# Kernel optimization log

Measured on AMD Instinct MI355X. Metric: run time of the kernel, lower is better.

## Reference

```python
import jax, jax.numpy as jnp
import numpy as np

N_NODES = 100000


def _mean_agg(x, src, dst, n_nodes):
    # mean of src-node features over in-edges of each dst node (DGL copy_u + mean)
    summed = jax.ops.segment_sum(x[src], dst, num_segments=n_nodes)  # [N, F]
    deg = jax.ops.segment_sum(jnp.ones_like(src, dtype=x.dtype), dst, num_segments=n_nodes)
    return summed / jnp.maximum(deg, 1.0)[:, None]  # nodes w/o in-edges -> 0


def _sage_conv(x, src, dst, W_self, W_neigh, b):
    # DGL SAGEConv('mean'): fc_self(h) + fc_neigh(mean_neigh(h)) + bias
    h_neigh = _mean_agg(x, src, dst, x.shape[0])
    return x @ W_self + h_neigh @ W_neigh + b


def setup_inputs() -> dict:
    key = jax.random.key(0)
    ks = jax.random.split(key, 8)
    F_IN, F_H, E = 128, 128, 1600000
    s = 1.0 / np.sqrt(F_IN)
    return {
        "x": jax.random.normal(ks[0], (N_NODES, F_IN), dtype=jnp.float32),
        "src": jax.random.randint(ks[1], (E,), 0, N_NODES, dtype=jnp.int64),
        "dst": jax.random.randint(ks[2], (E,), 0, N_NODES, dtype=jnp.int64),
        "W1_self": jax.random.normal(ks[3], (F_IN, F_H), dtype=jnp.float32) * s,
        "W1_neigh": jax.random.normal(ks[4], (F_IN, F_H), dtype=jnp.float32) * s,
        "b1": jnp.zeros((F_H,), dtype=jnp.float32),
        "W2_self": jax.random.normal(ks[5], (F_H, F_H), dtype=jnp.float32) * s,
        "W2_neigh": jax.random.normal(ks[6], (F_H, F_H), dtype=jnp.float32) * s,
        "b2": jnp.zeros((F_H,), dtype=jnp.float32),
    }


def reference(x, src, dst, W1_self, W1_neigh, b1, W2_self, W2_neigh, b2):
    h = _sage_conv(x, src, dst, W1_self, W1_neigh, b1)
    # dropout in eval mode == identity
    h = jax.nn.relu(h)
    return _sage_conv(h, src, dst, W2_self, W2_neigh, b2)
```

## Files before the change

### kernel.cpp

```cpp
#include <hip/hip_runtime.h>

#define F 128
#define NN 100000
#define NBUK 782
#define NBLK 256
#define LD 136
#define N4 (NN * F / 4)
#define N4A (N4 / 2)
#define SORT_CAP 8192

typedef __attribute__((ext_vector_type(8))) short short8;
typedef __attribute__((ext_vector_type(4))) float f32x4;
typedef __attribute__((ext_vector_type(2))) float f32x2;
typedef __attribute__((ext_vector_type(4))) int int4v;
typedef __attribute__((ext_vector_type(2))) int int2v;
typedef __attribute__((ext_vector_type(4))) unsigned short us4;
typedef unsigned short ushort_t;
typedef unsigned char uchar_t;

__device__ __forceinline__ ushort_t f2b(float f) {
    union { float f; unsigned u; } x;
    x.f = f;
    unsigned r = x.u + 0x7fffu + ((x.u >> 16) & 1u);
    return (ushort_t)(r >> 16);
}
__device__ __forceinline__ float b2f(ushort_t u) {
    union { unsigned u; float f; } x;
    x.u = ((unsigned)u) << 16;
    return x.f;
}

__device__ __forceinline__ unsigned f_to_e4m3(float v) {
    union { float f; unsigned b; } x; x.f = v;
    unsigned s = (x.b >> 24) & 0x80u;
    float a = fabsf(v);
    if (!(a < 448.f)) return s | 0x7Eu;
    if (a < 0.015625f) return s | (unsigned)__float2int_rn(a * 512.f);
    unsigned ab = x.b & 0x7FFFFFFFu;
    unsigned r = ab + 0x7FFFFu + ((ab >> 20) & 1u);
    unsigned e = (r >> 23) - 120u;
    return s | ((e << 3) | ((r >> 20) & 7u));
}
__device__ __forceinline__ float e4m3_to_f(unsigned u) {
    unsigned s = (u & 0x80u) << 24;
    unsigned e = (u >> 3) & 15u;
    unsigned m = u & 7u;
    union { unsigned b; float f; } x;
    x.b = s | ((e + 120u) << 23) | (m << 20);
    float f = x.f;
    if (e == 0) f = fmaf(f, 2.f, s ? 0.015625f : -0.015625f);
    return f;
}
__device__ __forceinline__ unsigned pack4_fp8(float f0, float f1, float f2, float f3) {
#if __has_builtin(__builtin_amdgcn_cvt_pk_fp8_f32)
    int w = 0;
    w = __builtin_amdgcn_cvt_pk_fp8_f32(f0, f1, w, false);
    w = __builtin_amdgcn_cvt_pk_fp8_f32(f2, f3, w, true);
    return (unsigned)w;
#else
    return f_to_e4m3(f0) | (f_to_e4m3(f1) << 8) | (f_to_e4m3(f2) << 16) |
           (f_to_e4m3(f3) << 24);
#endif
}
__device__ __forceinline__ void dec4(int w, float* o) {
#if __has_builtin(__builtin_amdgcn_cvt_pk_f32_fp8)
    f32x2 a = __builtin_amdgcn_cvt_pk_f32_fp8(w, false);
    f32x2 b = __builtin_amdgcn_cvt_pk_f32_fp8(w, true);
    o[0] = a[0]; o[1] = a[1]; o[2] = b[0]; o[3] = b[1];
#else
    o[0] = e4m3_to_f((unsigned)w & 0xFFu);
    o[1] = e4m3_to_f(((unsigned)w >> 8) & 0xFFu);
    o[2] = e4m3_to_f(((unsigned)w >> 16) & 0xFFu);
    o[3] = e4m3_to_f(((unsigned)w >> 24) & 0xFFu);
#endif
}

__device__ __forceinline__ int4v ld_row16(const ushort_t* p) {
    int4v r;
    asm volatile("global_load_dwordx4 %0, %1, off" : "=v"(r) : "v"(p) : "memory");
    return r;
}
__device__ __forceinline__ int2v ld_row8(const uchar_t* p) {
    int2v r;
    asm volatile("global_load_dwordx2 %0, %1, off" : "=v"(r) : "v"(p) : "memory");
    return r;
}

__global__ __launch_bounds__(256) void k1_fused(
    const int* __restrict__ dst, int* __restrict__ H, int E, int chunk,
    const float* __restrict__ Wa, const float* __restrict__ Wb,
    const float* __restrict__ Wc, const float* __restrict__ Wd,
    ushort_t* __restrict__ Oa, ushort_t* __restrict__ Ob,
    ushort_t* __restrict__ Oc, ushort_t* __restrict__ Od,
    const float* __restrict__ X, ushort_t* __restrict__ Y,
    uchar_t* __restrict__ X8) {
    __shared__ union {
        int h[NBUK];
        float tile[32][33];
    } u;
    const int blk = blockIdx.x;
    if (blk < NBLK) {
        for (int i = threadIdx.x; i < NBUK; i += 256) u.h[i] = 0;
        __syncthreads();
        const int s0 = blk * chunk, s1 = min(E, s0 + chunk);
        for (int i = s0 + threadIdx.x; i < s1; i += 256)
            atomicAdd(&u.h[dst[i] >> 7], 1);
        __syncthreads();
        for (int i = threadIdx.x; i < NBUK; i += 256)
            H[blk * NBUK + i] = u.h[i];
    } else if (blk < NBLK + 64) {
        const int m = (blk - NBLK) >> 4;
        const int b = (blk - NBLK) & 15;
        const float* W = (m == 0) ? Wa : (m == 1) ? Wb : (m == 2) ? Wc : Wd;
        ushort_t* WT = (m == 0) ? Oa : (m == 1) ? Ob : (m == 2) ? Oc : Od;
        const int by = (b >> 2) * 32;
        const int bx = (b & 3) * 32;
        const int tx = threadIdx.x & 31, ty = threadIdx.x >> 5;
        for (int i = 0; i < 32; i += 8)
            u.tile[ty + i][tx] = W[(by + ty + i) * F + bx + tx];
        __syncthreads();
        for (int i = 0; i < 32; i += 8)
            WT[(bx + ty + i) * F + by + tx] = f2b(u.tile[tx][ty + i]);
    } else {
        const int i = (blk - NBLK - 64) * 256 + threadIdx.x;
        if (i < N4A) {
            float4 v = ((const float4*)X)[i];
            us4 o;
            o.x = f2b(v.x); o.y = f2b(v.y); o.z = f2b(v.z); o.w = f2b(v.w);
            ((us4*)Y)[i] = o;
            ((unsigned*)X8)[i] = pack4_fp8(v.x, v.y, v.z, v.w);
        }
    }
}

__global__ __launch_bounds__(256) void scan_cols(int* __restrict__ H,
                                                 int* __restrict__ Htot) {
    __shared__ int s[NBLK];
    const int k = blockIdx.x;
    const int t = threadIdx.x;
    const int v = H[t * NBUK + k];
    s[t] = v;
    __syncthreads();
    for (int d = 1; d < NBLK; d <<= 1) {
        const int u = (t >= d) ? s[t - d] : 0;
        __syncthreads();
        s[t] += u;
        __syncthreads();
    }
    H[t * NBUK + k] = s[t] - v;
    if (t == NBLK - 1) Htot[k] = s[t];
}

__global__ __launch_bounds__(1024) void k2_fused(
    const int* __restrict__ Htot, int* __restrict__ boffs, int E,
    const float* __restrict__ X, ushort_t* __restrict__ Y,
    uchar_t* __restrict__ X8) {
    if (blockIdx.x == 0) {
        __shared__ int tot[1024];
        const int k = threadIdx.x;
        const int v = (k < NBUK) ? Htot[k] : 0;
        tot[k] = v;
        __syncthreads();
        for (int d = 1; d < 1024; d <<= 1) {
            const int u = (k >= d) ? tot[k - d] : 0;
            __syncthreads();
            tot[k] += u;
            __syncthreads();
        }
        if (k < NBUK) boffs[k] = tot[k] - v;
        if (k == 0) boffs[NBUK] = E;
    } else {
        const int i = N4A + (blockIdx.x - 1) * 1024 + threadIdx.x;
        if (i < N4) {
            float4 v = ((const float4*)X)[i];
            us4 o;
            o.x = f2b(v.x); o.y = f2b(v.y); o.z = f2b(v.z); o.w = f2b(v.w);
            ((us4*)Y)[i] = o;
            ((unsigned*)X8)[i] = pack4_fp8(v.x, v.y, v.z, v.w);
        }
    }
}

__global__ __launch_bounds__(256) void scatter2(const int* __restrict__ src,
                                                const int* __restrict__ dst,
                                                const int* __restrict__ H,
                                                const int* __restrict__ boffs,
                                                unsigned* __restrict__ pairs,
                                                int E, int chunk) {
    __shared__ int cur[NBUK];
    const int b = blockIdx.x;
    for (int i = threadIdx.x; i < NBUK; i += 256)
        cur[i] = boffs[i] + H[b * NBUK + i];
    __syncthreads();
    const int s0 = b * chunk, s1 = min(E, s0 + chunk);
    for (int i = s0 + threadIdx.x; i < s1; i += 256) {
        const int d = dst[i];
        const int p = atomicAdd(&cur[d >> 7], 1);
        pairs[p] = ((unsigned)(d & 127) << 20) | (unsigned)src[i];
    }
}

__global__ __launch_bounds__(256) void bucket_sort(const unsigned* __restrict__ pairs,
                                                   const int* __restrict__ boffs,
                                                   int* __restrict__ offs,
                                                   int* __restrict__ csr) {
    __shared__ int cnt[128], loffs[128], lcur[128];
    __shared__ unsigned sbuf[SORT_CAP];
    const int b = blockIdx.x, t = threadIdx.x;
    const int e0 = boffs[b], e1 = boffs[b + 1];
    const int n = e1 - e0;
    const int node0 = b << 7;
    const int nnode = min(128, NN - node0);
    if (t < 128) cnt[t] = 0;
    __syncthreads();
    for (int i = e0 + t; i < e1; i += 256) atomicAdd(&cnt[pairs[i] >> 20], 1);
    __syncthreads();
    if (t < 128) loffs[t] = cnt[t];
    __syncthreads();
    for (int d = 1; d < 128; d <<= 1) {
        int u = (t >= d && t < 128) ? loffs[t - d] : 0;
        __syncthreads();
        if (t < 128) loffs[t] += u;
        __syncthreads();
    }
    if (t < 128) {
        const int ex = loffs[t] - cnt[t];
        lcur[t] = ex;
        if (t < nnode) offs[node0 + t] = e0 + ex;
    }
    if (b == NBUK - 1 && t == 0) offs[NN] = e1;
    __syncthreads();

    if (n <= SORT_CAP) {
        for (int i = e0 + t; i < e1; i += 256) {
            const unsigned v = pairs[i];
            const int p = atomicAdd(&lcur[v >> 20], 1);
            sbuf[p] = v;
        }
        __syncthreads();
        for (int i = t; i < n; i += 256) {
            const unsigned v = sbuf[i];
            const int d = v >> 20;
            const int hi = loffs[d];
            const int lo = hi - cnt[d];
            int r = lo;
            for (int j = lo; j < hi; ++j) {
                const unsigned w = sbuf[j];
                r += (w < v) || (w == v && j < i);
            }
            csr[e0 + r] = (int)(v & 0xFFFFFu);
        }
    } else {
        for (int i = e0 + t; i < e1; i += 256) {
            const unsigned v = pairs[i];
            const int p = atomicAdd(&lcur[v >> 20], 1);
            csr[e0 + p] = (int)(v & 0xFFFFFu);
        }
    }
}

template <typename TOUT, int GF8>
__global__ __launch_bounds__(256) void sage_layer(
    const ushort_t* __restrict__ Xg, const uchar_t* __restrict__ X8g,
    const int* __restrict__ offs, const int* __restrict__ csr,
    const ushort_t* __restrict__ WTs, const ushort_t* __restrict__ WTn,
    const float* __restrict__ bias,
    TOUT* __restrict__ out, uchar_t* __restrict__ out8, int relu) {
    __shared__ __align__(16) ushort_t sX[32 * LD];
    __shared__ __align__(16) ushort_t sH[32 * LD];
    const int t = threadIdx.x;
    const int lane = t & 63;
    const int wave = t >> 6;
    const int brow0 = blockIdx.x * 32;

    {
        const ushort_t* base = Xg + (size_t)brow0 * F;
        for (int i = t; i < 32 * 16; i += 256) {
            int row = i >> 4, ch = i & 15;
            *(short8*)&sX[row * LD + ch * 8] = *(const short8*)&base[row * F + ch * 8];
        }
    }

    {
        const int slot = lane >> 4;
        const int cl = lane & 15;
        const int c8 = cl * 8;
#pragma unroll
        for (int rr = 0; rr < 2; rr++) {
            const int rloc = wave * 8 + slot * 2 + rr;
            const int row = brow0 + rloc;
            const int e0 = offs[row], e1 = offs[row + 1];
            const int d = e1 - e0;
            float acc[8];
#pragma unroll
            for (int j = 0; j < 8; j++) acc[j] = 0.f;
            if (d > 0) {
                const int e1m1 = e1 - 1;
                if constexpr (GF8) {
                    const int nb = (d + 15) >> 4;
#pragma unroll 1
                    for (int b = 0; b < nb; b++) {
                        const int e = e0 + b * 16;
#define IDX9(K) const int i##K = csr[min(e + K, e1m1)];
                        IDX9(0) IDX9(1) IDX9(2) IDX9(3) IDX9(4) IDX9(5) IDX9(6) IDX9(7)
                        IDX9(8) IDX9(9) IDX9(10) IDX9(11) IDX9(12) IDX9(13) IDX9(14) IDX9(15)
#undef IDX9
#define LDR9(K) int2v r##K = ld_row8(X8g + (size_t)i##K * F + c8);
                        LDR9(0) LDR9(1) LDR9(2) LDR9(3) LDR9(4) LDR9(5) LDR9(6) LDR9(7)
                        LDR9(8) LDR9(9) LDR9(10) LDR9(11) LDR9(12) LDR9(13) LDR9(14) LDR9(15)
#undef LDR9
                        asm volatile("s_waitcnt vmcnt(0)" ::: "memory");
                        asm volatile("" : "+v"(r0), "+v"(r1), "+v"(r2), "+v"(r3),
                                           "+v"(r4), "+v"(r5), "+v"(r6), "+v"(r7),
                                           "+v"(r8), "+v"(r9), "+v"(r10), "+v"(r11),
                                           "+v"(r12), "+v"(r13), "+v"(r14), "+v"(r15));
                        __builtin_amdgcn_sched_barrier(0);
#define ACC9(K) { float tv[8]; dec4(r##K.x, tv); dec4(r##K.y, tv + 4);            \
                  const float mk = (e + K < e1) ? 1.f : 0.f;                      \
                  _Pragma("unroll")                                               \
                  for (int j = 0; j < 8; j++) acc[j] = fmaf(mk, tv[j], acc[j]); }
                        ACC9(0) ACC9(1) ACC9(2) ACC9(3) ACC9(4) ACC9(5) ACC9(6) ACC9(7)
                        ACC9(8) ACC9(9) ACC9(10) ACC9(11) ACC9(12) ACC9(13) ACC9(14) ACC9(15)
#undef ACC9
                    }
                } else {
                    const int nb = (d + 7) >> 3;
#pragma unroll 1
                    for (int b = 0; b < nb; b++) {
                        const int e = e0 + b * 8;
                        const int i0 = csr[e];
                        const int i1 = csr[min(e + 1, e1m1)];
                        const int i2 = csr[min(e + 2, e1m1)];
                        const int i3 = csr[min(e + 3, e1m1)];
                        const int i4 = csr[min(e + 4, e1m1)];
                        const int i5 = csr[min(e + 5, e1m1)];
                        const int i6 = csr[min(e + 6, e1m1)];
                        const int i7 = csr[min(e + 7, e1m1)];
                        int4v r0 = ld_row16(Xg + (size_t)i0 * F + c8);
                        int4v r1 = ld_row16(Xg + (size_t)i1 * F + c8);
                        int4v r2 = ld_row16(Xg + (size_t)i2 * F + c8);
                        int4v r3 = ld_row16(Xg + (size_t)i3 * F + c8);
                        int4v r4 = ld_row16(Xg + (size_t)i4 * F + c8);
                        int4v r5 = ld_row16(Xg + (size_t)i5 * F + c8);
                        int4v r6 = ld_row16(Xg + (size_t)i6 * F + c8);
                        int4v r7 = ld_row16(Xg + (size_t)i7 * F + c8);
                        asm volatile("s_waitcnt vmcnt(0)" ::: "memory");
                        asm volatile("" : "+v"(r0), "+v"(r1), "+v"(r2), "+v"(r3),
                                           "+v"(r4), "+v"(r5), "+v"(r6), "+v"(r7));
                        __builtin_amdgcn_sched_barrier(0);
                        const short8 v0 = __builtin_bit_cast(short8, r0);
                        const short8 v1 = __builtin_bit_cast(short8, r1);
                        const short8 v2 = __builtin_bit_cast(short8, r2);
                        const short8 v3 = __builtin_bit_cast(short8, r3);
                        const short8 v4 = __builtin_bit_cast(short8, r4);
                        const short8 v5 = __builtin_bit_cast(short8, r5);
                        const short8 v6 = __builtin_bit_cast(short8, r6);
                        const short8 v7 = __builtin_bit_cast(short8, r7);
                        const float m1 = (e + 1 < e1) ? 1.f : 0.f;
                        const float m2 = (e + 2 < e1) ? 1.f : 0.f;
                        const float m3 = (e + 3 < e1) ? 1.f : 0.f;
                        const float m4 = (e + 4 < e1) ? 1.f : 0.f;
                        const float m5 = (e + 5 < e1) ? 1.f : 0.f;
                        const float m6 = (e + 6 < e1) ? 1.f : 0.f;
                        const float m7 = (e + 7 < e1) ? 1.f : 0.f;
#pragma unroll
                        for (int j = 0; j < 8; j++) {
                            float s01 = b2f((ushort_t)v0[j]) + m1 * b2f((ushort_t)v1[j]);
                            float s23 = m2 * b2f((ushort_t)v2[j]) + m3 * b2f((ushort_t)v3[j]);
                            float s45 = m4 * b2f((ushort_t)v4[j]) + m5 * b2f((ushort_t)v5[j]);
                            float s67 = m6 * b2f((ushort_t)v6[j]) + m7 * b2f((ushort_t)v7[j]);
                            acc[j] += (s01 + s23) + (s45 + s67);
                        }
                    }
                }
            }
            const float inv = (d > 0) ? (1.0f / (float)d) : 0.f;
            short8 o;
#pragma unroll
            for (int j = 0; j < 8; j++) o[j] = (short)f2b(acc[j] * inv);
            *(short8*)&sH[rloc * LD + c8] = o;
        }
    }
    __syncthreads();

    const int q = lane >> 4, nl = lane & 15;
    const int colbase = wave * 32;
    f32x4 acc00 = (f32x4)0.f, acc01 = (f32x4)0.f, acc10 = (f32x4)0.f, acc11 = (f32x4)0.f;
#pragma unroll
    for (int ks = 0; ks < 4; ks++) {
        const int ko = ks * 32 + q * 8;
        const short8 aS0 = *(const short8*)&sX[nl * LD + ko];
        const short8 aS1 = *(const short8*)&sX[(16 + nl) * LD + ko];
        const short8 aN0 = *(const short8*)&sH[nl * LD + ko];
        const short8 aN1 = *(const short8*)&sH[(16 + nl) * LD + ko];
        const size_t bo0 = (size_t)(colbase + nl) * F + ko;
        const size_t bo1 = (size_t)(colbase + 16 + nl) * F + ko;
        const short8 bS0 = *(const short8*)&WTs[bo0];
        const short8 bS1 = *(const short8*)&WTs[bo1];
        const short8 bN0 = *(const short8*)&WTn[bo0];
        const short8 bN1 = *(const short8*)&WTn[bo1];
        acc00 = __builtin_amdgcn_mfma_f32_16x16x32_bf16(aS0, bS0, acc00, 0, 0, 0);
        acc00 = __builtin_amdgcn_mfma_f32_16x16x32_bf16(aN0, bN0, acc00, 0, 0, 0);
        acc01 = __builtin_amdgcn_mfma_f32_16x16x32_bf16(aS0, bS1, acc01, 0, 0, 0);
        acc01 = __builtin_amdgcn_mfma_f32_16x16x32_bf16(aN0, bN1, acc01, 0, 0, 0);
        acc10 = __builtin_amdgcn_mfma_f32_16x16x32_bf16(aS1, bS0, acc10, 0, 0, 0);
        acc10 = __builtin_amdgcn_mfma_f32_16x16x32_bf16(aN1, bN0, acc10, 0, 0, 0);
        acc11 = __builtin_amdgcn_mfma_f32_16x16x32_bf16(aS1, bS1, acc11, 0, 0, 0);
        acc11 = __builtin_amdgcn_mfma_f32_16x16x32_bf16(aN1, bN1, acc11, 0, 0, 0);
    }

    const float b0 = bias[colbase + nl];
    const float b1 = bias[colbase + 16 + nl];
    if constexpr (sizeof(TOUT) == 2) {
        __syncthreads();
#pragma unroll
        for (int r = 0; r < 4; r++) {
            const int lr0 = q * 4 + r, lr1 = 16 + q * 4 + r;
            float v00 = acc00[r] + b0, v01 = acc01[r] + b1;
            float v10 = acc10[r] + b0, v11 = acc11[r] + b1;
            if (relu) {
                v00 = fmaxf(v00, 0.f); v01 = fmaxf(v01, 0.f);
                v10 = fmaxf(v10, 0.f); v11 = fmaxf(v11, 0.f);
            }
            sX[lr0 * LD + colbase + nl] = f2b(v00);
            sX[lr0 * LD + colbase + 16 + nl] = f2b(v01);
            sX[lr1 * LD + colbase + nl] = f2b(v10);
            sX[lr1 * LD + colbase + 16 + nl] = f2b(v11);
        }
        __syncthreads();
        TOUT* base = out + (size_t)brow0 * F;
        for (int i = t; i < 32 * 16; i += 256) {
            int row = i >> 4, ch = i & 15;
            const short8 v = *(const short8*)&sX[row * LD + ch * 8];
            *(short8*)&base[row * F + ch * 8] = v;
            if (out8) {
                float f[8];
#pragma unroll
                for (int j = 0; j < 8; j++) f[j] = b2f((ushort_t)v[j]);
                int2v p;
                p.x = (int)pack4_fp8(f[0], f[1], f[2], f[3]);
                p.y = (int)pack4_fp8(f[4], f[5], f[6], f[7]);
                *(int2v*)&out8[(size_t)(brow0 + row) * F + ch * 8] = p;
            }
        }
    } else {
#pragma unroll
        for (int r = 0; r < 4; r++) {
            const int orow0 = brow0 + q * 4 + r;
            const int orow1 = brow0 + 16 + q * 4 + r;
            float v00 = acc00[r] + b0, v01 = acc01[r] + b1;
            float v10 = acc10[r] + b0, v11 = acc11[r] + b1;
            if (relu) {
                v00 = fmaxf(v00, 0.f); v01 = fmaxf(v01, 0.f);
                v10 = fmaxf(v10, 0.f); v11 = fmaxf(v11, 0.f);
            }
            out[(size_t)orow0 * F + colbase + nl] = v00;
            out[(size_t)orow0 * F + colbase + 16 + nl] = v01;
            out[(size_t)orow1 * F + colbase + nl] = v10;
            out[(size_t)orow1 * F + colbase + 16 + nl] = v11;
        }
    }
}

extern "C" void kernel_launch(void* const* d_in, const int* in_sizes, int n_in,
                              void* d_out, int out_size, void* d_ws, size_t ws_size,
                              hipStream_t stream) {
    const float* x = (const float*)d_in[0];
    const int* src = (const int*)d_in[1];
    const int* dst = (const int*)d_in[2];
    const float* W1s = (const float*)d_in[3];
    const float* W1n = (const float*)d_in[4];
    const float* b1 = (const float*)d_in[5];
    const float* W2s = (const float*)d_in[6];
    const float* W2n = (const float*)d_in[7];
    const float* b2 = (const float*)d_in[8];
    float* out = (float*)d_out;

    const int E = in_sizes[1];
    const int N = NN;
    const int E4 = (E + 3) & ~3;
    const int chunk = (E + NBLK - 1) / NBLK;

    unsigned* pairs = (unsigned*)d_ws;
    int* csr = (int*)(pairs + E4);
    ushort_t* h1 = (ushort_t*)(csr + E4);
    ushort_t* WT1s = h1 + (size_t)N * F;
    ushort_t* WT1n = WT1s + F * F;
    ushort_t* WT2s = WT1n + F * F;
    ushort_t* WT2n = WT2s + F * F;
    int* offs = (int*)(WT2n + F * F);
    int* H = offs + (N + 1);
    int* boffs = H + NBLK * NBUK;
    int* Htot = boffs + (NBUK + 1);
    ushort_t* xb = (ushort_t*)d_out;
    uchar_t* x8 = (uchar_t*)d_out + (size_t)N * F * 2;
    size_t off8 = (size_t)((char*)(Htot + NBUK) - (char*)d_ws);
    off8 = (off8 + 7) & ~(size_t)7;
    uchar_t* h1f8 = (uchar_t*)d_ws + off8;
    const bool l2f8 = ws_size >= off8 + (size_t)N * F;

    const int cvtA_blocks = (N4A + 255) / 256;
    k1_fused<<<NBLK + 64 + cvtA_blocks, 256, 0, stream>>>(
        dst, H, E, chunk, W1s, W1n, W2s, W2n, WT1s, WT1n, WT2s, WT2n, x, xb, x8);
    scan_cols<<<NBUK, NBLK, 0, stream>>>(H, Htot);
    const int cvtB_blocks = (N4 - N4A + 1023) / 1024;
    k2_fused<<<1 + cvtB_blocks, 1024, 0, stream>>>(Htot, boffs, E, x, xb, x8);
    scatter2<<<NBLK, 256, 0, stream>>>(src, dst, H, boffs, pairs, E, chunk);
    bucket_sort<<<NBUK, 256, 0, stream>>>(pairs, boffs, offs, csr);

    sage_layer<ushort_t, 1><<<N / 32, 256, 0, stream>>>(
        xb, x8, offs, csr, WT1s, WT1n, b1, h1, l2f8 ? h1f8 : nullptr, 1);
    if (l2f8) {
        sage_layer<float, 1><<<N / 32, 256, 0, stream>>>(
            h1, h1f8, offs, csr, WT2s, WT2n, b2, out, nullptr, 0);
    } else {
        sage_layer<float, 0><<<N / 32, 256, 0, stream>>>(
            h1, nullptr, offs, csr, WT2s, WT2n, b2, out, nullptr, 0);
    }
}
```

Measured before the change: 334.6 us.

## Fold bucket-offset scan into scatter and move all conversion into k1

Removes the k2_fused kernel. Each scatter2 block now redundantly computes the exclusive scan of bucket totals itself, and block 0 writes boffs for the later sort. The x to bf16/fp8 conversion is done entirely in k1_fused, with each block converting two float4 elements per thread. This saves one kernel launch and a dependency step, at the cost of a redundant per-block scan and a larger first kernel.

```diff
diff --git a/kernel.cpp b/kernel.cpp
--- a/kernel.cpp
+++ b/kernel.cpp
@@ -6,7 +6,6 @@
 #define NBLK 256
 #define LD 136
 #define N4 (NN * F / 4)
-#define N4A (N4 / 2)
 #define SORT_CAP 8192
 
 typedef __attribute__((ext_vector_type(8))) short short8;
@@ -122,13 +121,17 @@
         for (int i = 0; i < 32; i += 8)
             WT[(bx + ty + i) * F + by + tx] = f2b(u.tile[tx][ty + i]);
     } else {
-        const int i = (blk - NBLK - 64) * 256 + threadIdx.x;
-        if (i < N4A) {
-            float4 v = ((const float4*)X)[i];
-            us4 o;
-            o.x = f2b(v.x); o.y = f2b(v.y); o.z = f2b(v.z); o.w = f2b(v.w);
-            ((us4*)Y)[i] = o;
-            ((unsigned*)X8)[i] = pack4_fp8(v.x, v.y, v.z, v.w);
+        const int base = (blk - NBLK - 64) * 512;
+#pragma unroll
+        for (int k = 0; k < 2; k++) {
+            const int i = base + k * 256 + threadIdx.x;
+            if (i < N4) {
+                float4 v = ((const float4*)X)[i];
+                us4 o;
+                o.x = f2b(v.x); o.y = f2b(v.y); o.z = f2b(v.z); o.w = f2b(v.w);
+                ((us4*)Y)[i] = o;
+                ((unsigned*)X8)[i] = pack4_fp8(v.x, v.y, v.z, v.w);
+            }
         }
     }
 }
@@ -151,49 +154,46 @@
     if (t == NBLK - 1) Htot[k] = s[t];
 }
 
-__global__ __launch_bounds__(1024) void k2_fused(
-    const int* __restrict__ Htot, int* __restrict__ boffs, int E,
-    const float* __restrict__ X, ushort_t* __restrict__ Y,
-    uchar_t* __restrict__ X8) {
-    if (blockIdx.x == 0) {
-        __shared__ int tot[1024];
-        const int k = threadIdx.x;
-        const int v = (k < NBUK) ? Htot[k] : 0;
-        tot[k] = v;
-        __syncthreads();
-        for (int d = 1; d < 1024; d <<= 1) {
-            const int u = (k >= d) ? tot[k - d] : 0;
-            __syncthreads();
-            tot[k] += u;
-            __syncthreads();
-        }
-        if (k < NBUK) boffs[k] = tot[k] - v;
-        if (k == 0) boffs[NBUK] = E;
-    } else {
-        const int i = N4A + (blockIdx.x - 1) * 1024 + threadIdx.x;
-        if (i < N4) {
-            float4 v = ((const float4*)X)[i];
-            us4 o;
-            o.x = f2b(v.x); o.y = f2b(v.y); o.z = f2b(v.z); o.w = f2b(v.w);
-            ((us4*)Y)[i] = o;
-            ((unsigned*)X8)[i] = pack4_fp8(v.x, v.y, v.z, v.w);
-        }
-    }
-}
-
 __global__ __launch_bounds__(256) void scatter2(const int* __restrict__ src,
                                                 const int* __restrict__ dst,
                                                 const int* __restrict__ H,
-                                                const int* __restrict__ boffs,
+                                                const int* __restrict__ Htot,
+                                                int* __restrict__ boffs,
                                                 unsigned* __restrict__ pairs,
                                                 int E, int chunk) {
     __shared__ int cur[NBUK];
+    __shared__ int part[256];
     const int b = blockIdx.x;
-    for (int i = threadIdx.x; i < NBUK; i += 256)
-        cur[i] = boffs[i] + H[b * NBUK + i];
+    const int t = threadIdx.x;
+    int v0 = 0, v1 = 0, v2 = 0, v3 = 0;
+    {
+        const int base = t * 4;
+        if (base + 0 < NBUK) v0 = Htot[base + 0];
+        if (base + 1 < NBUK) v1 = Htot[base + 1];
+        if (base + 2 < NBUK) v2 = Htot[base + 2];
+        if (base + 3 < NBUK) v3 = Htot[base + 3];
+    }
+    const int own = v0 + v1 + v2 + v3;
+    part[t] = own;
+    __syncthreads();
+    for (int d = 1; d < 256; d <<= 1) {
+        const int u = (t >= d) ? part[t - d] : 0;
+        __syncthreads();
+        part[t] += u;
+        __syncthreads();
+    }
+    {
+        int run = part[t] - own;
+        const int base = t * 4;
+        if (base + 0 < NBUK) { cur[base + 0] = run + H[b * NBUK + base + 0]; if (b == 0) boffs[base + 0] = run; run += v0; }
+        if (base + 1 < NBUK) { cur[base + 1] = run + H[b * NBUK + base + 1]; if (b == 0) boffs[base + 1] = run; run += v1; }
+        if (base + 2 < NBUK) { cur[base + 2] = run + H[b * NBUK + base + 2]; if (b == 0) boffs[base + 2] = run; run += v2; }
+        if (base + 3 < NBUK) { cur[base + 3] = run + H[b * NBUK + base + 3]; if (b == 0) boffs[base + 3] = run; run += v3; }
+    }
+    if (b == 0 && t == 0) boffs[NBUK] = E;
     __syncthreads();
     const int s0 = b * chunk, s1 = min(E, s0 + chunk);
-    for (int i = s0 + threadIdx.x; i < s1; i += 256) {
+    for (int i = s0 + t; i < s1; i += 256) {
         const int d = dst[i];
         const int p = atomicAdd(&cur[d >> 7], 1);
         pairs[p] = ((unsigned)(d & 127) << 20) | (unsigned)src[i];
@@ -499,13 +499,11 @@
     uchar_t* h1f8 = (uchar_t*)d_ws + off8;
     const bool l2f8 = ws_size >= off8 + (size_t)N * F;
 
-    const int cvtA_blocks = (N4A + 255) / 256;
-    k1_fused<<<NBLK + 64 + cvtA_blocks, 256, 0, stream>>>(
+    const int cvt_blocks = (N4 + 511) / 512;
+    k1_fused<<<NBLK + 64 + cvt_blocks, 256, 0, stream>>>(
         dst, H, E, chunk, W1s, W1n, W2s, W2n, WT1s, WT1n, WT2s, WT2n, x, xb, x8);
     scan_cols<<<NBUK, NBLK, 0, stream>>>(H, Htot);
-    const int cvtB_blocks = (N4 - N4A + 1023) / 1024;
-    k2_fused<<<1 + cvtB_blocks, 1024, 0, stream>>>(Htot, boffs, E, x, xb, x8);
-    scatter2<<<NBLK, 256, 0, stream>>>(src, dst, H, boffs, pairs, E, chunk);
+    scatter2<<<NBLK, 256, 0, stream>>>(src, dst, H, Htot, boffs, pairs, E, chunk);
     bucket_sort<<<NBUK, 256, 0, stream>>>(pairs, boffs, offs, csr);
 
     sage_layer<ushort_t, 1><<<N / 32, 256, 0, stream>>>(
```

After: 332.6 us, median of 2. No clear change (-0.6%).
